# Performance work log

Measured on AMD Instinct MI355X. Metric: run time of the kernel, lower is better.

## Reference

```python
import jax, jax.numpy as jnp
import numpy as np

N, E, IN, HID, OUT = 100000, 1600000, 128, 128, 64


def _gcn(x, w, b, src, dst, norm, n):
    # PyG GCNConv: linear transform, then normalized scatter-add aggregation
    h = x @ w                                  # [N, F_out]
    msg = h[src] * norm[:, None]               # gather + scale, [E', F_out]
    agg = jax.ops.segment_sum(msg, dst, num_segments=n)
    return agg + b


def setup_inputs() -> dict:
    key = jax.random.key(0)
    ks = jax.random.split(key, 10)
    s = 0.05
    return {
        "X": jax.random.normal(ks[0], (N, IN), jnp.float32),
        "edge_index": jax.random.randint(ks[1], (2, E), 0, N, jnp.int64),
        "unused": 0,
        "gw1": jax.random.normal(ks[2], (IN, HID), jnp.float32) * s,
        "gb1": jnp.zeros((HID,), jnp.float32),
        "lw1": jax.random.normal(ks[3], (IN, HID), jnp.float32) * s,
        "lb1": jnp.zeros((HID,), jnp.float32),
        "gw2": jax.random.normal(ks[4], (HID, HID), jnp.float32) * s,
        "gb2": jnp.zeros((HID,), jnp.float32),
        "lw2": jax.random.normal(ks[5], (HID, HID), jnp.float32) * s,
        "lb2": jnp.zeros((HID,), jnp.float32),
        "gw3": jax.random.normal(ks[6], (HID, HID), jnp.float32) * s,
        "gb3": jnp.zeros((HID,), jnp.float32),
        "lw3": jax.random.normal(ks[7], (HID, HID), jnp.float32) * s,
        "lb3": jnp.zeros((HID,), jnp.float32),
        "fcw": jax.random.normal(ks[8], (HID, OUT), jnp.float32) * s,
        "fcb": jnp.zeros((OUT,), jnp.float32),
    }


def reference(X, edge_index, unused, gw1, gb1, lw1, lb1, gw2, gb2, lw2, lb2,
              gw3, gb3, lw3, lb3, fcw, fcb):
    n = X.shape[0]
    loop = jnp.arange(n)
    src = jnp.concatenate([edge_index[0], loop])   # self-loops appended
    dst = jnp.concatenate([edge_index[1], loop])
    deg = jax.ops.segment_sum(jnp.ones_like(dst, dtype=X.dtype), dst, num_segments=n)
    dis = jnp.where(deg > 0, jax.lax.rsqrt(jnp.maximum(deg, 1e-12)), 0.0)
    norm = dis[src] * dis[dst]                     # D^-1/2 (A+I) D^-1/2 weights

    lrelu = lambda v: jax.nn.leaky_relu(v, negative_slope=0.01)
    h = lrelu(_gcn(X, gw1, gb1, src, dst, norm, n) + X @ lw1 + lb1)
    h = lrelu(_gcn(h, gw2, gb2, src, dst, norm, n) + h @ lw2 + lb2)
    h = lrelu(_gcn(h, gw3, gb3, src, dst, norm, n) + h @ lw3 + lb3)
    y = h @ fcw + fcb
    return (h, y)
```

## Files before the change

kernel.cpp:

```cpp
#include <hip/hip_runtime.h>
#include <cstdint>
#include <cstddef>


typedef __attribute__((ext_vector_type(4))) float f32x4;
typedef __attribute__((ext_vector_type(8))) short bf16x8;
typedef unsigned short u16;

#define G_CHUNKS 256

__device__ __forceinline__ float bf2f(unsigned int u) {
  union { unsigned int i; float f; } v;
  v.i = u << 16;
  return v.f;
}
__device__ __forceinline__ u16 f2bf(float f) {
  union { float f; unsigned int i; } v;
  v.f = f;
  unsigned int i = v.i;
  return (u16)((i + 0x7FFFu + ((i >> 16) & 1u)) >> 16);
}


__global__ __launch_bounds__(256) void k_hist(const int* __restrict__ ei,
                                              int* __restrict__ ghist,
                                              int E, int B, int chunk) {
  __shared__ int h[512];
  for (int t = threadIdx.x; t < B; t += 256) h[t] = 0;
  __syncthreads();
  const int g = blockIdx.x;
  const int beg = g * chunk;
  const int end = min(beg + chunk, E);
  for (int e = beg + threadIdx.x; e < end; e += 256)
    atomicAdd(&h[ei[E + e] >> 8], 1);
  __syncthreads();
  for (int t = threadIdx.x; t < B; t += 256) ghist[(size_t)t * G_CHUNKS + g] = h[t];
}

__global__ __launch_bounds__(256) void k_hscan(int* __restrict__ ghist,
                                               int* __restrict__ btot) {
  __shared__ int sm[256];
  int* p = ghist + (size_t)blockIdx.x * G_CHUNKS;
  const int t = threadIdx.x;
  int v = p[t];
  sm[t] = v;
  __syncthreads();
  for (int off = 1; off < 256; off <<= 1) {
    int u = (t >= off) ? sm[t - off] : 0;
    __syncthreads();
    sm[t] += u;
    __syncthreads();
  }
  p[t] = sm[t] - v;
  if (t == 255) btot[blockIdx.x] = sm[255];
}

__global__ __launch_bounds__(512) void k_bscan(const int* __restrict__ btot,
                                               int* __restrict__ boff, int B,
                                               int* __restrict__ rowptr, int n,
                                               int E, int tot) {
  __shared__ int sm[512];
  const int t = threadIdx.x;
  int v = (t < B) ? btot[t] : 0;
  sm[t] = v;
  __syncthreads();
  for (int off = 1; off < 512; off <<= 1) {
    int u = (t >= off) ? sm[t - off] : 0;
    __syncthreads();
    sm[t] += u;
    __syncthreads();
  }
  if (t < B) boff[t] = sm[t] - v;
  if (t == 0) {
    boff[B] = E;
    rowptr[n] = tot;
  }
}

__global__ __launch_bounds__(256) void k_scatter(const int* __restrict__ ei,
                                                 const int* __restrict__ ghist,
                                                 const int* __restrict__ boff,
                                                 unsigned int* __restrict__ ebuf,
                                                 int E, int B, int chunk) {
  __shared__ int off[512];
  const int g = blockIdx.x;
  for (int t = threadIdx.x; t < B; t += 256)
    off[t] = boff[t] + ghist[(size_t)t * G_CHUNKS + g];
  __syncthreads();
  const int beg = g * chunk;
  const int end = min(beg + chunk, E);
  for (int e = beg + threadIdx.x; e < end; e += 256) {
    int s = ei[e];
    int d = ei[E + e];
    int pos = atomicAdd(&off[d >> 8], 1);
    ebuf[pos] = ((unsigned int)s << 8) | (unsigned int)(d & 255);
  }
}

__global__ __launch_bounds__(256) void k_cfill(const unsigned int* __restrict__ ebuf,
                                               const int* __restrict__ boff,
                                               int* __restrict__ rowptr,
                                               int* __restrict__ col,
                                               float* __restrict__ dis,
                                               float* __restrict__ idis, int n) {
  __shared__ int cnt[256];
  __shared__ int fl[256];
  const int b = blockIdx.x;
  const int t = threadIdx.x;
  const int beg = boff[b];
  const int end = boff[b + 1];
  const int node0 = b << 8;
  const int nn = min(256, n - node0);
  cnt[t] = 0;
  __syncthreads();
  for (int e = beg + t; e < end; e += 256)
    atomicAdd(&cnt[ebuf[e] & 255u], 1);
  __syncthreads();
  int v = cnt[t];
  __shared__ int sm[256];
  sm[t] = v;
  __syncthreads();
  for (int off = 1; off < 256; off <<= 1) {
    int u = (t >= off) ? sm[t - off] : 0;
    __syncthreads();
    sm[t] += u;
    __syncthreads();
  }
  if (t < nn) {
    int excl = sm[t] - v;
    int rbase = beg + node0 + t + excl;
    int i = node0 + t;
    rowptr[i] = rbase;
    col[rbase] = i;
    fl[t] = rbase + 1;
    float dv = (float)(v + 1);
    dis[i] = rsqrtf(dv);
    idis[i] = sqrtf(dv);
  }
  __syncthreads();
  for (int e = beg + t; e < end; e += 256) {
    unsigned int pk = ebuf[e];
    int pos = atomicAdd(&fl[pk & 255u], 1);
    col[pos] = (int)(pk >> 8);
  }
}


__global__ __launch_bounds__(256) void k_cvt(const float* __restrict__ src,
                                             const float* __restrict__ dis,
                                             u16* __restrict__ dsts, int total8) {
  int i = blockIdx.x * 256 + threadIdx.x;
  if (i >= total8) return;
  size_t b = (size_t)i * 8;
  float ds = dis[i >> 4];
  float4 a0 = *(const float4*)(src + b);
  float4 a1 = *(const float4*)(src + b + 4);
  u16 os[8] = {f2bf(a0.x * ds), f2bf(a0.y * ds), f2bf(a0.z * ds), f2bf(a0.w * ds),
               f2bf(a1.x * ds), f2bf(a1.y * ds), f2bf(a1.z * ds), f2bf(a1.w * ds)};
  *(ulonglong2*)(dsts + b) = *(ulonglong2*)os;
}

__global__ __launch_bounds__(128) void k_prep(const float* __restrict__ w0,
                                              const float* __restrict__ w1,
                                              const float* __restrict__ w2,
                                              const float* __restrict__ w3,
                                              const float* __restrict__ w4,
                                              const float* __restrict__ w5,
                                              const float* __restrict__ g1,
                                              const float* __restrict__ l1,
                                              const float* __restrict__ g2,
                                              const float* __restrict__ l2,
                                              const float* __restrict__ g3,
                                              const float* __restrict__ l3,
                                              const float* __restrict__ fcw,
                                              u16* __restrict__ wt,
                                              float* __restrict__ bias,
                                              u16* __restrict__ fcT) {
  int bx = blockIdx.x;
  if (bx < 768) {
    int z = bx >> 7, nr = bx & 127, k = threadIdx.x;
    const float* Ws[6] = {w0, w1, w2, w3, w4, w5};
    wt[(size_t)z * 16384 + nr * 128 + k] = f2bf(Ws[z][k * 128 + nr]);
  } else if (bx < 771) {
    int t = (bx - 768) * 128 + threadIdx.x;
    if (t < 384) {
      const float* gs[3] = {g1, g2, g3};
      const float* ls[3] = {l1, l2, l3};
      bias[t] = gs[t >> 7][t & 127] + ls[t >> 7][t & 127];
    }
  } else {
    int nr = bx - 771;
    int k = threadIdx.x;
    fcT[nr * 128 + k] = f2bf(fcw[k * 64 + nr]);
  }
}

__global__ __launch_bounds__(256, 8) void k_spmv_bf(const int* __restrict__ rowptr,
                                                    const int* __restrict__ col,
                                                    const float* __restrict__ dis,
                                                    const u16* __restrict__ Xs,
                                                    u16* __restrict__ SXb, int n) {
  const int tid = threadIdx.x;
  const int half = (tid >> 5) & 1;
  const int sub = tid & 31;
  const int i = blockIdx.x * 8 + (tid >> 6) * 2 + half;
  if (i >= n) return;
  int j = rowptr[i];
  const int end = rowptr[i + 1];
  float a0 = 0.f, a1 = 0.f, a2 = 0.f, a3 = 0.f;

#define ROWQ(c) (*(const uint2*)(Xs + (size_t)(c) * 128 + sub * 4))
#define ACC(q)  do { uint2 _q = (q); \
                     a0 += bf2f(_q.x & 0xffffu); a1 += bf2f(_q.x >> 16); \
                     a2 += bf2f(_q.y & 0xffffu); a3 += bf2f(_q.y >> 16); } while (0)

  for (; (j & 3) && j < end; ++j) ACC(ROWQ(col[j]));
  for (; j + 7 < end; j += 8) {
    int4 c0 = *(const int4*)(col + j);
    int4 c1 = *(const int4*)(col + j + 4);
    uint2 q0 = ROWQ(c0.x), q1 = ROWQ(c0.y), q2 = ROWQ(c0.z), q3 = ROWQ(c0.w);
    uint2 q4 = ROWQ(c1.x), q5 = ROWQ(c1.y), q6 = ROWQ(c1.z), q7 = ROWQ(c1.w);
    ACC(q0); ACC(q1); ACC(q2); ACC(q3);
    ACC(q4); ACC(q5); ACC(q6); ACC(q7);
  }
  if (j + 3 < end) {
    int4 c0 = *(const int4*)(col + j);
    uint2 q0 = ROWQ(c0.x), q1 = ROWQ(c0.y), q2 = ROWQ(c0.z), q3 = ROWQ(c0.w);
    ACC(q0); ACC(q1); ACC(q2); ACC(q3);
    j += 4;
  }
  for (; j < end; ++j) ACC(ROWQ(col[j]));
#undef ROWQ
#undef ACC

  const float di = dis[i];
  uint2 o;
  o.x = (unsigned int)f2bf(a0 * di) | ((unsigned int)f2bf(a1 * di) << 16);
  o.y = (unsigned int)f2bf(a2 * di) | ((unsigned int)f2bf(a3 * di) << 16);
  *(uint2*)(SXb + (size_t)i * 128 + sub * 4) = o;
}

__global__ __launch_bounds__(256, 8) void k_mfma(const u16* __restrict__ A0,
                                                 const u16* __restrict__ A1s,
                                                 const u16* __restrict__ W0T,
                                                 const u16* __restrict__ W1T,
                                                 const float* __restrict__ bias,
                                                 const float* __restrict__ dis,
                                                 const float* __restrict__ idis,
                                                 u16* __restrict__ outs,
                                                 float* __restrict__ outf, int M) {
  const int lane = threadIdx.x & 63;
  const int wv = threadIdx.x >> 6;
  const int row0 = blockIdx.x * 128 + wv * 32;
  const int c0off = blockIdx.y * 32;
  const int r = lane & 15;
  const int kg = lane >> 4;

  f32x4 accA[2][2], accB[2][2];
#pragma unroll
  for (int a = 0; a < 2; ++a)
#pragma unroll
    for (int j = 0; j < 2; ++j) {
      accA[a][j] = (f32x4){0.f, 0.f, 0.f, 0.f};
      accB[a][j] = (f32x4){0.f, 0.f, 0.f, 0.f};
    }

  const int ra0 = min(row0 + r, M - 1);
  const int ra1 = min(row0 + 16 + r, M - 1);

#pragma unroll
  for (int kk = 0; kk < 4; ++kk) {
    const int k0 = kk * 32 + kg * 8;
    bf16x8 a0 = *(const bf16x8*)(A0 + (size_t)ra0 * 128 + k0);
    bf16x8 a1 = *(const bf16x8*)(A0 + (size_t)ra1 * 128 + k0);
#pragma unroll
    for (int j = 0; j < 2; ++j) {
      bf16x8 b = *(const bf16x8*)(W0T + (size_t)(c0off + j * 16 + r) * 128 + k0);
      accA[0][j] = __builtin_amdgcn_mfma_f32_16x16x32_bf16(a0, b, accA[0][j], 0, 0, 0);
      accA[1][j] = __builtin_amdgcn_mfma_f32_16x16x32_bf16(a1, b, accA[1][j], 0, 0, 0);
    }
  }
#pragma unroll
  for (int kk = 0; kk < 4; ++kk) {
    const int k0 = kk * 32 + kg * 8;
    bf16x8 a0 = *(const bf16x8*)(A1s + (size_t)ra0 * 128 + k0);
    bf16x8 a1 = *(const bf16x8*)(A1s + (size_t)ra1 * 128 + k0);
#pragma unroll
    for (int j = 0; j < 2; ++j) {
      bf16x8 b = *(const bf16x8*)(W1T + (size_t)(c0off + j * 16 + r) * 128 + k0);
      accB[0][j] = __builtin_amdgcn_mfma_f32_16x16x32_bf16(a0, b, accB[0][j], 0, 0, 0);
      accB[1][j] = __builtin_amdgcn_mfma_f32_16x16x32_bf16(a1, b, accB[1][j], 0, 0, 0);
    }
  }

#pragma unroll
  for (int rf = 0; rf < 2; ++rf)
#pragma unroll
    for (int e = 0; e < 4; ++e) {
      const int row = row0 + rf * 16 + kg * 4 + e;
      if (row >= M) continue;
      const float ids = idis[row];
      const float ds = dis[row];
#pragma unroll
      for (int j = 0; j < 2; ++j) {
        const int c = c0off + j * 16 + r;
        float v = accA[rf][j][e] + ids * accB[rf][j][e] + bias[c];
        v = (v > 0.f) ? v : 0.01f * v;
        if (outf) outf[(size_t)row * 128 + c] = v;
        if (outs) outs[(size_t)row * 128 + c] = f2bf(v * ds);
      }
    }
}

__global__ __launch_bounds__(256) void k_fc_mfma(const u16* __restrict__ hs3,
                                                 const u16* __restrict__ fcT,
                                                 const float* __restrict__ fcb,
                                                 const float* __restrict__ idis,
                                                 float* __restrict__ y, int M) {
  const int lane = threadIdx.x & 63;
  const int wv = threadIdx.x >> 6;
  const int row0 = blockIdx.x * 128 + wv * 32;
  const int r = lane & 15;
  const int kg = lane >> 4;

  f32x4 acc[2][4];
#pragma unroll
  for (int a = 0; a < 2; ++a)
#pragma unroll
    for (int j = 0; j < 4; ++j) acc[a][j] = (f32x4){0.f, 0.f, 0.f, 0.f};

  const int ra0 = min(row0 + r, M - 1);
  const int ra1 = min(row0 + 16 + r, M - 1);

#pragma unroll
  for (int kk = 0; kk < 4; ++kk) {
    const int k0 = kk * 32 + kg * 8;
    bf16x8 a0 = *(const bf16x8*)(hs3 + (size_t)ra0 * 128 + k0);
    bf16x8 a1 = *(const bf16x8*)(hs3 + (size_t)ra1 * 128 + k0);
#pragma unroll
    for (int j = 0; j < 4; ++j) {
      bf16x8 b = *(const bf16x8*)(fcT + (size_t)(j * 16 + r) * 128 + k0);
      acc[0][j] = __builtin_amdgcn_mfma_f32_16x16x32_bf16(a0, b, acc[0][j], 0, 0, 0);
      acc[1][j] = __builtin_amdgcn_mfma_f32_16x16x32_bf16(a1, b, acc[1][j], 0, 0, 0);
    }
  }

#pragma unroll
  for (int rf = 0; rf < 2; ++rf)
#pragma unroll
    for (int e = 0; e < 4; ++e) {
      const int row = row0 + rf * 16 + kg * 4 + e;
      if (row >= M) continue;
      const float ids = idis[row];
#pragma unroll
      for (int j = 0; j < 4; ++j) {
        const int c = j * 16 + r;
        y[(size_t)row * 64 + c] = ids * acc[rf][j][e] + fcb[c];
      }
    }
}


extern "C" void kernel_launch(void* const* d_in, const int* in_sizes, int n_in,
                              void* d_out, int out_size, void* d_ws, size_t ws_size,
                              hipStream_t stream) {
  const float* X  = (const float*)d_in[0];
  const int* ei   = (const int*)d_in[1];
  const float* gw1 = (const float*)d_in[3];
  const float* gb1 = (const float*)d_in[4];
  const float* lw1 = (const float*)d_in[5];
  const float* lb1 = (const float*)d_in[6];
  const float* gw2 = (const float*)d_in[7];
  const float* gb2 = (const float*)d_in[8];
  const float* lw2 = (const float*)d_in[9];
  const float* lb2 = (const float*)d_in[10];
  const float* gw3 = (const float*)d_in[11];
  const float* gb3 = (const float*)d_in[12];
  const float* lw3 = (const float*)d_in[13];
  const float* lb3 = (const float*)d_in[14];
  const float* fcw = (const float*)d_in[15];
  const float* fcb = (const float*)d_in[16];

  const int n = in_sizes[0] / 128;
  const int E = in_sizes[1] / 2;
  const int tot = E + n;
  const int B = (n + 255) >> 8;
  const int chunk = (E + G_CHUNKS - 1) / G_CHUNKS;

  char* ws = (char*)d_ws;
  size_t off = 0;
  auto alloc = [&](size_t bytes) -> void* {
    void* p = ws + off;
    off = (off + bytes + 255) & ~(size_t)255;
    return p;
  };
  int* ghist   = (int*)alloc((size_t)B * G_CHUNKS * 4);
  int* btot    = (int*)alloc(512 * 4);
  int* boff    = (int*)alloc((size_t)(B + 1) * 4);
  int* rowptr  = (int*)alloc((size_t)(n + 1) * 4);
  float* dis   = (float*)alloc((size_t)n * 4);
  float* idis  = (float*)alloc((size_t)n * 4);
  int* col     = (int*)alloc((size_t)tot * 4);
  unsigned int* ebuf = (unsigned int*)alloc((size_t)E * 4);
  u16* Xs      = (u16*)alloc((size_t)n * 128 * 2);
  u16* SXb     = (u16*)alloc((size_t)n * 128 * 2);
  u16* WT      = (u16*)alloc((size_t)6 * 16384 * 2);
  u16* fcT     = (u16*)alloc((size_t)64 * 128 * 2);
  float* bias  = (float*)alloc(384 * 4);

  float* outh = (float*)d_out;
  float* outy = outh + (size_t)n * 128;
  u16* hb = (u16*)outy;

  const int gM = (n + 127) / 128;
  const int gW = (n + 7) / 8;
  const int g8 = (n * 128 / 8 + 255) / 256;

  k_hist<<<G_CHUNKS, 256, 0, stream>>>(ei, ghist, E, B, chunk);
  k_hscan<<<B, 256, 0, stream>>>(ghist, btot);
  k_bscan<<<1, 512, 0, stream>>>(btot, boff, B, rowptr, n, E, tot);
  k_scatter<<<G_CHUNKS, 256, 0, stream>>>(ei, ghist, boff, ebuf, E, B, chunk);
  k_cfill<<<B, 256, 0, stream>>>(ebuf, boff, rowptr, col, dis, idis, n);

  k_cvt<<<g8, 256, 0, stream>>>(X, dis, Xs, n * 128 / 8);
  k_prep<<<835, 128, 0, stream>>>(gw1, lw1, gw2, lw2, gw3, lw3,
                                  gb1, lb1, gb2, lb2, gb3, lb3, fcw,
                                  WT, bias, fcT);

  k_spmv_bf<<<gW, 256, 0, stream>>>(rowptr, col, dis, Xs, SXb, n);
  k_mfma<<<dim3(gM, 4), 256, 0, stream>>>(SXb, Xs, WT, WT + 16384, bias,
                                          dis, idis, hb, nullptr, n);
  k_spmv_bf<<<gW, 256, 0, stream>>>(rowptr, col, dis, hb, SXb, n);
  k_mfma<<<dim3(gM, 4), 256, 0, stream>>>(SXb, hb, WT + 2 * 16384, WT + 3 * 16384,
                                          bias + 128, dis, idis, Xs, nullptr, n);
  k_spmv_bf<<<gW, 256, 0, stream>>>(rowptr, col, dis, Xs, SXb, n);
  k_mfma<<<dim3(gM, 4), 256, 0, stream>>>(SXb, Xs, WT + 4 * 16384, WT + 5 * 16384,
                                          bias + 256, dis, idis, hb, outh, n);
  k_fc_mfma<<<gM, 256, 0, stream>>>(hb, fcT, fcb, idis, outy, n);
}
```

Baseline: 446.6 us.

## Fuse SpMV aggregation and MFMA transform into one per-layer kernel

Merges the sparse aggregation kernel and the dual-GEMM MFMA kernel into a single k_layer kernel. Each 512-thread block aggregates 16 nodes into XOR-swizzled LDS as bf16, then 8 waves each compute 16 output columns with MFMA, reading the aggregated tile from LDS. This removes the SXb intermediate round-trip through global memory and three kernel launches. The cost is smaller GEMM tiles, with weights re-read per 16-row block and the self term read from global per block, and a block-wide barrier that ties MFMA work to the slowest node's gather.

```diff
diff --git a/kernel.cpp b/kernel.cpp
--- a/kernel.cpp
+++ b/kernel.cpp
@@ -195,121 +195,96 @@
   }
 }
 
-__global__ __launch_bounds__(256, 8) void k_spmv_bf(const int* __restrict__ rowptr,
-                                                    const int* __restrict__ col,
-                                                    const float* __restrict__ dis,
-                                                    const u16* __restrict__ Xs,
-                                                    u16* __restrict__ SXb, int n) {
+__global__ __launch_bounds__(512, 8) void k_layer(const int* __restrict__ rowptr,
+                                                  const int* __restrict__ col,
+                                                  const float* __restrict__ dis,
+                                                  const float* __restrict__ idis,
+                                                  const u16* __restrict__ As,
+                                                  const u16* __restrict__ W0T,
+                                                  const u16* __restrict__ W1T,
+                                                  const float* __restrict__ bias,
+                                                  u16* __restrict__ outs,
+                                                  float* __restrict__ outf,
+                                                  int n) {
+  __shared__ char ldsb[16 * 256];
   const int tid = threadIdx.x;
-  const int half = (tid >> 5) & 1;
-  const int sub = tid & 31;
-  const int i = blockIdx.x * 8 + (tid >> 6) * 2 + half;
-  if (i >= n) return;
-  int j = rowptr[i];
-  const int end = rowptr[i + 1];
-  float a0 = 0.f, a1 = 0.f, a2 = 0.f, a3 = 0.f;
-
-#define ROWQ(c) (*(const uint2*)(Xs + (size_t)(c) * 128 + sub * 4))
+
+  {
+    const int nodeLocal = tid >> 5;
+    const int sub = tid & 31;
+    const int i = blockIdx.x * 16 + nodeLocal;
+    float a0 = 0.f, a1 = 0.f, a2 = 0.f, a3 = 0.f;
+    if (i < n) {
+      int j = rowptr[i];
+      const int end = rowptr[i + 1];
+
+#define ROWQ(c) (*(const uint2*)(As + (size_t)(c) * 128 + sub * 4))
 #define ACC(q)  do { uint2 _q = (q); \
                      a0 += bf2f(_q.x & 0xffffu); a1 += bf2f(_q.x >> 16); \
                      a2 += bf2f(_q.y & 0xffffu); a3 += bf2f(_q.y >> 16); } while (0)
 
-  for (; (j & 3) && j < end; ++j) ACC(ROWQ(col[j]));
-  for (; j + 7 < end; j += 8) {
-    int4 c0 = *(const int4*)(col + j);
-    int4 c1 = *(const int4*)(col + j + 4);
-    uint2 q0 = ROWQ(c0.x), q1 = ROWQ(c0.y), q2 = ROWQ(c0.z), q3 = ROWQ(c0.w);
-    uint2 q4 = ROWQ(c1.x), q5 = ROWQ(c1.y), q6 = ROWQ(c1.z), q7 = ROWQ(c1.w);
-    ACC(q0); ACC(q1); ACC(q2); ACC(q3);
-    ACC(q4); ACC(q5); ACC(q6); ACC(q7);
-  }
-  if (j + 3 < end) {
-    int4 c0 = *(const int4*)(col + j);
-    uint2 q0 = ROWQ(c0.x), q1 = ROWQ(c0.y), q2 = ROWQ(c0.z), q3 = ROWQ(c0.w);
-    ACC(q0); ACC(q1); ACC(q2); ACC(q3);
-    j += 4;
-  }
-  for (; j < end; ++j) ACC(ROWQ(col[j]));
+      for (; (j & 3) && j < end; ++j) ACC(ROWQ(col[j]));
+      for (; j + 7 < end; j += 8) {
+        int4 c0 = *(const int4*)(col + j);
+        int4 c1 = *(const int4*)(col + j + 4);
+        uint2 q0 = ROWQ(c0.x), q1 = ROWQ(c0.y), q2 = ROWQ(c0.z), q3 = ROWQ(c0.w);
+        uint2 q4 = ROWQ(c1.x), q5 = ROWQ(c1.y), q6 = ROWQ(c1.z), q7 = ROWQ(c1.w);
+        ACC(q0); ACC(q1); ACC(q2); ACC(q3);
+        ACC(q4); ACC(q5); ACC(q6); ACC(q7);
+      }
+      if (j + 3 < end) {
+        int4 c0 = *(const int4*)(col + j);
+        uint2 q0 = ROWQ(c0.x), q1 = ROWQ(c0.y), q2 = ROWQ(c0.z), q3 = ROWQ(c0.w);
+        ACC(q0); ACC(q1); ACC(q2); ACC(q3);
+        j += 4;
+      }
+      for (; j < end; ++j) ACC(ROWQ(col[j]));
 #undef ROWQ
 #undef ACC
 
-  const float di = dis[i];
-  uint2 o;
-  o.x = (unsigned int)f2bf(a0 * di) | ((unsigned int)f2bf(a1 * di) << 16);
-  o.y = (unsigned int)f2bf(a2 * di) | ((unsigned int)f2bf(a3 * di) << 16);
-  *(uint2*)(SXb + (size_t)i * 128 + sub * 4) = o;
-}
-
-__global__ __launch_bounds__(256, 8) void k_mfma(const u16* __restrict__ A0,
-                                                 const u16* __restrict__ A1s,
-                                                 const u16* __restrict__ W0T,
-                                                 const u16* __restrict__ W1T,
-                                                 const float* __restrict__ bias,
-                                                 const float* __restrict__ dis,
-                                                 const float* __restrict__ idis,
-                                                 u16* __restrict__ outs,
-                                                 float* __restrict__ outf, int M) {
-  const int lane = threadIdx.x & 63;
-  const int wv = threadIdx.x >> 6;
-  const int row0 = blockIdx.x * 128 + wv * 32;
-  const int c0off = blockIdx.y * 32;
+      const float di = dis[i];
+      a0 *= di; a1 *= di; a2 *= di; a3 *= di;
+    }
+    uint2 o;
+    o.x = (unsigned int)f2bf(a0) | ((unsigned int)f2bf(a1) << 16);
+    o.y = (unsigned int)f2bf(a2) | ((unsigned int)f2bf(a3) << 16);
+    *(uint2*)(ldsb + nodeLocal * 256 + ((sub * 8) ^ (nodeLocal << 4))) = o;
+  }
+  __syncthreads();
+
+  const int lane = tid & 63;
+  const int wv = tid >> 6;
+  const int c0off = wv * 16;
   const int r = lane & 15;
   const int kg = lane >> 4;
-
-  f32x4 accA[2][2], accB[2][2];
-#pragma unroll
-  for (int a = 0; a < 2; ++a)
-#pragma unroll
-    for (int j = 0; j < 2; ++j) {
-      accA[a][j] = (f32x4){0.f, 0.f, 0.f, 0.f};
-      accB[a][j] = (f32x4){0.f, 0.f, 0.f, 0.f};
-    }
-
-  const int ra0 = min(row0 + r, M - 1);
-  const int ra1 = min(row0 + 16 + r, M - 1);
+  const int grow = blockIdx.x * 16;
+  const int ra = min(grow + r, n - 1);
+
+  f32x4 accA = (f32x4){0.f, 0.f, 0.f, 0.f};
+  f32x4 accB = (f32x4){0.f, 0.f, 0.f, 0.f};
 
 #pragma unroll
   for (int kk = 0; kk < 4; ++kk) {
     const int k0 = kk * 32 + kg * 8;
-    bf16x8 a0 = *(const bf16x8*)(A0 + (size_t)ra0 * 128 + k0);
-    bf16x8 a1 = *(const bf16x8*)(A0 + (size_t)ra1 * 128 + k0);
-#pragma unroll
-    for (int j = 0; j < 2; ++j) {
-      bf16x8 b = *(const bf16x8*)(W0T + (size_t)(c0off + j * 16 + r) * 128 + k0);
-      accA[0][j] = __builtin_amdgcn_mfma_f32_16x16x32_bf16(a0, b, accA[0][j], 0, 0, 0);
-      accA[1][j] = __builtin_amdgcn_mfma_f32_16x16x32_bf16(a1, b, accA[1][j], 0, 0, 0);
-    }
-  }
-#pragma unroll
-  for (int kk = 0; kk < 4; ++kk) {
-    const int k0 = kk * 32 + kg * 8;
-    bf16x8 a0 = *(const bf16x8*)(A1s + (size_t)ra0 * 128 + k0);
-    bf16x8 a1 = *(const bf16x8*)(A1s + (size_t)ra1 * 128 + k0);
-#pragma unroll
-    for (int j = 0; j < 2; ++j) {
-      bf16x8 b = *(const bf16x8*)(W1T + (size_t)(c0off + j * 16 + r) * 128 + k0);
-      accB[0][j] = __builtin_amdgcn_mfma_f32_16x16x32_bf16(a0, b, accB[0][j], 0, 0, 0);
-      accB[1][j] = __builtin_amdgcn_mfma_f32_16x16x32_bf16(a1, b, accB[1][j], 0, 0, 0);
-    }
-  }
-
-#pragma unroll
-  for (int rf = 0; rf < 2; ++rf)
-#pragma unroll
-    for (int e = 0; e < 4; ++e) {
-      const int row = row0 + rf * 16 + kg * 4 + e;
-      if (row >= M) continue;
-      const float ids = idis[row];
-      const float ds = dis[row];
-#pragma unroll
-      for (int j = 0; j < 2; ++j) {
-        const int c = c0off + j * 16 + r;
-        float v = accA[rf][j][e] + ids * accB[rf][j][e] + bias[c];
-        v = (v > 0.f) ? v : 0.01f * v;
-        if (outf) outf[(size_t)row * 128 + c] = v;
-        if (outs) outs[(size_t)row * 128 + c] = f2bf(v * ds);
-      }
-    }
+    const int kb = (k0 * 2) ^ (r << 4);
+    bf16x8 aA = *(const bf16x8*)(ldsb + r * 256 + kb);
+    bf16x8 aB = *(const bf16x8*)(As + (size_t)ra * 128 + k0);
+    bf16x8 b0 = *(const bf16x8*)(W0T + (size_t)(c0off + r) * 128 + k0);
+    bf16x8 b1 = *(const bf16x8*)(W1T + (size_t)(c0off + r) * 128 + k0);
+    accA = __builtin_amdgcn_mfma_f32_16x16x32_bf16(aA, b0, accA, 0, 0, 0);
+    accB = __builtin_amdgcn_mfma_f32_16x16x32_bf16(aB, b1, accB, 0, 0, 0);
+  }
+
+#pragma unroll
+  for (int e = 0; e < 4; ++e) {
+    const int row = grow + kg * 4 + e;
+    if (row >= n) continue;
+    const int c = c0off + r;
+    float v = accA[e] + idis[row] * accB[e] + bias[c];
+    v = (v > 0.f) ? v : 0.01f * v;
+    if (outf) outf[(size_t)row * 128 + c] = v;
+    if (outs) outs[(size_t)row * 128 + c] = f2bf(v * dis[row]);
+  }
 }
 
 __global__ __launch_bounds__(256) void k_fc_mfma(const u16* __restrict__ hs3,
@@ -403,7 +378,6 @@
   int* col     = (int*)alloc((size_t)tot * 4);
   unsigned int* ebuf = (unsigned int*)alloc((size_t)E * 4);
   u16* Xs      = (u16*)alloc((size_t)n * 128 * 2);
-  u16* SXb     = (u16*)alloc((size_t)n * 128 * 2);
   u16* WT      = (u16*)alloc((size_t)6 * 16384 * 2);
   u16* fcT     = (u16*)alloc((size_t)64 * 128 * 2);
   float* bias  = (float*)alloc(384 * 4);
@@ -413,7 +387,7 @@
   u16* hb = (u16*)outy;
 
   const int gM = (n + 127) / 128;
-  const int gW = (n + 7) / 8;
+  const int gL = (n + 15) / 16;
   const int g8 = (n * 128 / 8 + 255) / 256;
 
   k_hist<<<G_CHUNKS, 256, 0, stream>>>(ei, ghist, E, B, chunk);
@@ -427,14 +401,13 @@
                                   gb1, lb1, gb2, lb2, gb3, lb3, fcw,
                                   WT, bias, fcT);
 
-  k_spmv_bf<<<gW, 256, 0, stream>>>(rowptr, col, dis, Xs, SXb, n);
-  k_mfma<<<dim3(gM, 4), 256, 0, stream>>>(SXb, Xs, WT, WT + 16384, bias,
-                                          dis, idis, hb, nullptr, n);
-  k_spmv_bf<<<gW, 256, 0, stream>>>(rowptr, col, dis, hb, SXb, n);
-  k_mfma<<<dim3(gM, 4), 256, 0, stream>>>(SXb, hb, WT + 2 * 16384, WT + 3 * 16384,
-                                          bias + 128, dis, idis, Xs, nullptr, n);
-  k_spmv_bf<<<gW, 256, 0, stream>>>(rowptr, col, dis, Xs, SXb, n);
-  k_mfma<<<dim3(gM, 4), 256, 0, stream>>>(SXb, Xs, WT + 4 * 16384, WT + 5 * 16384,
-                                          bias + 256, dis, idis, hb, outh, n);
+  k_layer<<<gL, 512, 0, stream>>>(rowptr, col, dis, idis, Xs,
+                                  WT, WT + 16384, bias, hb, nullptr, n);
+  k_layer<<<gL, 512, 0, stream>>>(rowptr, col, dis, idis, hb,
+                                  WT + 2 * 16384, WT + 3 * 16384, bias + 128,
+                                  Xs, nullptr, n);
+  k_layer<<<gL, 512, 0, stream>>>(rowptr, col, dis, idis, Xs,
+                                  WT + 4 * 16384, WT + 5 * 16384, bias + 256,
+                                  hb, outh, n);
   k_fc_mfma<<<gM, 256, 0, stream>>>(hb, fcT, fcb, idis, outy, n);
 }
```

Result: slower. 490.2 us (+9.8%).
